# Performance work log

Hardware: AMD Instinct MI355X
Metric: run time of the kernel (lower is better)

## Reference

```python
import jax, jax.numpy as jnp
import numpy as np

B, S, V, D, F, H, L = 2, 1024, 32000, 768, 3072, 12, 6
DH = D // H


def layer_norm(x, g, b, eps=1e-5):
    mu = jnp.mean(x, axis=-1, keepdims=True)
    var = jnp.mean((x - mu) ** 2, axis=-1, keepdims=True)
    return (x - mu) / jnp.sqrt(var + eps) * g + b


def setup_inputs() -> dict:
    key = jax.random.key(0)
    ks = jax.random.split(key, 20)
    s = 0.02  # init scale
    p = {
        'x': jax.random.randint(ks[0], (B, S), 0, V),
        'tok_emb': jax.random.normal(ks[1], (V, D), jnp.float32) * s,
        'pos_emb': jax.random.normal(ks[2], (S, D), jnp.float32) * s,
        'Wq': jax.random.normal(ks[3], (L, D, D), jnp.float32) * s,
        'bq': jnp.zeros((L, D), jnp.float32),
        'Wk': jax.random.normal(ks[4], (L, D, D), jnp.float32) * s,
        'bk': jnp.zeros((L, D), jnp.float32),
        'Wv': jax.random.normal(ks[5], (L, D, D), jnp.float32) * s,
        'bv': jnp.zeros((L, D), jnp.float32),
        'Wo': jax.random.normal(ks[6], (L, D, D), jnp.float32) * s,
        'bo': jnp.zeros((L, D), jnp.float32),
        'ln1_g': jnp.ones((L, D), jnp.float32),
        'ln1_b': jnp.zeros((L, D), jnp.float32),
        'W1': jax.random.normal(ks[7], (L, D, F), jnp.float32) * s,
        'b1': jnp.zeros((L, F), jnp.float32),
        'W2': jax.random.normal(ks[8], (L, F, D), jnp.float32) * s,
        'b2': jnp.zeros((L, D), jnp.float32),
        'ln2_g': jnp.ones((L, D), jnp.float32),
        'ln2_b': jnp.zeros((L, D), jnp.float32),
        'Wf': jax.random.normal(ks[9], (D, V), jnp.float32) * s,
        'bf': jnp.zeros((V,), jnp.float32),
    }
    return p


def reference(x, tok_emb, pos_emb, Wq, bq, Wk, bk, Wv, bv, Wo, bo,
              ln1_g, ln1_b, W1, b1, W2, b2, ln2_g, ln2_b, Wf, bf):
    hset = tok_emb[x] + pos_emb[None, :x.shape[1], :]  # [B,S,D]
    scale = 1.0 / jnp.sqrt(jnp.float32(D))  # note: original scales by sqrt(d_k)=sqrt(d_model)
    for i in range(L):
        q = (hset @ Wq[i] + bq[i]).reshape(B, S, H, DH).transpose(0, 2, 1, 3)
        k = (hset @ Wk[i] + bk[i]).reshape(B, S, H, DH).transpose(0, 2, 1, 3)
        v = (hset @ Wv[i] + bv[i]).reshape(B, S, H, DH).transpose(0, 2, 1, 3)
        scores = jnp.einsum('bhqd,bhkd->bhqk', q, k) * scale
        probs = jax.nn.softmax(scores, axis=-1)
        o = jnp.einsum('bhqk,bhkd->bhqd', probs, v)
        o = o.transpose(0, 2, 1, 3).reshape(B, S, D)
        attn = o @ Wo[i] + bo[i]
        h1 = layer_norm(attn + hset, ln1_g[i], ln1_b[i])
        ff = jax.nn.gelu(h1 @ W1[i] + b1[i], approximate=False) @ W2[i] + b2[i]
        hset = layer_norm(ff + h1, ln2_g[i], ln2_b[i])
    logits = hset @ Wf + bf
    log_probs = jax.nn.log_softmax(logits, axis=-1)
    return (log_probs, hset)
```

## Files before the change

kernel.cpp:

```cpp
#include <hip/hip_runtime.h>
#include <hip/hip_bf16.h>
#include <math.h>

#define B_ 2
#define S_ 1024
#define V_ 32000
#define D_ 768
#define F_ 3072
#define H_ 12
#define L_ 6
#define DH_ 64
#define BS_ (B_*S_)
#define NQKV_ 2304
#define KVB_ 128

typedef __attribute__((ext_vector_type(8))) short short8;
typedef __attribute__((ext_vector_type(4))) float f32x4;

__device__ __forceinline__ unsigned short f2b(float f) {
    union { __hip_bfloat16 h; unsigned short u; } cv;
    cv.h = __float2bfloat16(f);
    return cv.u;
}

__device__ __forceinline__ void store_bf4(__hip_bfloat16* p, float a, float b, float c, float d) {
    unsigned long long pk = (unsigned long long)f2b(a)
        | ((unsigned long long)f2b(b) << 16)
        | ((unsigned long long)f2b(c) << 32)
        | ((unsigned long long)f2b(d) << 48);
    *(unsigned long long*)p = pk;
}

__device__ __forceinline__ void gld16(const void* g, void* l) {
    __builtin_amdgcn_global_load_lds(
        (const __attribute__((address_space(1))) unsigned int*)g,
        (__attribute__((address_space(3))) unsigned int*)l,
        16, 0, 0);
}

__global__ void embed_k(const int* __restrict__ x, const float* __restrict__ tok,
                        const float* __restrict__ pos, float* __restrict__ h,
                        __hip_bfloat16* __restrict__ hbf) {
    int bs = blockIdx.x;
    int s = bs % S_;
    int t = x[bs];
    for (int d = threadIdx.x; d < D_; d += blockDim.x) {
        float v = tok[(size_t)t * D_ + d] + pos[(size_t)s * D_ + d];
        h[(size_t)bs * D_ + d] = v;
        hbf[(size_t)bs * D_ + d] = __float2bfloat16(v);
    }
}

__global__ __launch_bounds__(256) void transp_k(const float* __restrict__ src, size_t sl,
                                                __hip_bfloat16* __restrict__ dst, size_t dl,
                                                int N, int K) {
    const float* S = src + (size_t)blockIdx.z * sl;
    __hip_bfloat16* Dp = dst + (size_t)blockIdx.z * dl;
    __shared__ float T[32][33];
    const int k0 = blockIdx.y * 32, n0 = blockIdx.x * 32;
    const int tid = threadIdx.x;
    const int r = tid >> 3, c4 = (tid & 7) * 4;
    float4 vv = *(const float4*)&S[(size_t)(k0 + r) * N + n0 + c4];
    T[r][c4 + 0] = vv.x; T[r][c4 + 1] = vv.y; T[r][c4 + 2] = vv.z; T[r][c4 + 3] = vv.w;
    __syncthreads();
    store_bf4(&Dp[(size_t)(n0 + r) * K + k0 + c4],
              T[c4 + 0][r], T[c4 + 1][r], T[c4 + 2][r], T[c4 + 3][r]);
}

__global__ void bcat_k(const float* __restrict__ bq, const float* __restrict__ bk,
                       const float* __restrict__ bv, float* __restrict__ dst) {
    int l = blockIdx.x;
    for (int j = threadIdx.x; j < D_; j += blockDim.x) {
        dst[(size_t)l * NQKV_ + j]          = bq[(size_t)l * D_ + j];
        dst[(size_t)l * NQKV_ + D_ + j]     = bk[(size_t)l * D_ + j];
        dst[(size_t)l * NQKV_ + 2 * D_ + j] = bv[(size_t)l * D_ + j];
    }
}

__global__ void cvt_k(const float* __restrict__ in, __hip_bfloat16* __restrict__ out, int n) {
    int i = (blockIdx.x * 256 + threadIdx.x) * 4;
    if (i < n) {
        float4 v = *(const float4*)&in[i];
        store_bf4(&out[i], v.x, v.y, v.z, v.w);
    }
}

template<int BM, int BN, int ACT, bool WF32, bool WBF, bool SW, bool XS, bool WVT>
__global__ __launch_bounds__(256) void mgemm_k(const __hip_bfloat16* __restrict__ A,
                                               const __hip_bfloat16* __restrict__ Bt,
                                               const float* __restrict__ bias,
                                               float* __restrict__ Cf,
                                               __hip_bfloat16* __restrict__ Cb,
                                               __hip_bfloat16* __restrict__ vTp,
                                               int M, int N, int K) {
    constexpr int WM = BM / 2, WN = BN / 2;
    constexpr int FM = WM / 16, FN = WN / 16;
    __shared__ __hip_bfloat16 Al[BM * 64];
    __shared__ __hip_bfloat16 Bl[BN * 64];
    const int tid = threadIdx.x;
    const int wid = tid >> 6, lane = tid & 63;
    const int wr = wid >> 1, wc = wid & 1;
    const int lrow = lane & 15, kq = lane >> 4;

    int bx = blockIdx.x, by = blockIdx.y;
    if (XS) {
        const int gx = gridDim.x;
        const int nwg = gx * gridDim.y;
        const int lin = by * gx + bx;
        const int logical = (lin & 7) * (nwg >> 3) + (lin >> 3);
        bx = logical % gx;
        by = logical / gx;
    }
    const int row0 = (SW ? bx : by) * BM;
    const int col0 = (SW ? by : bx) * BN;

    f32x4 acc[FM][FN];
    #pragma unroll
    for (int i = 0; i < FM; ++i)
        #pragma unroll
        for (int j = 0; j < FN; ++j)
            acc[i][j] = (f32x4){0.f, 0.f, 0.f, 0.f};

    const int srow = (lane >> 3);
    const int scol = ((lane & 7) ^ srow) * 8;

    for (int kk = 0; kk < K; kk += 64) {
        #pragma unroll
        for (int i = 0; i < BM / 32; ++i)
            gld16(A + (size_t)(row0 + i * 32 + wid * 8 + srow) * K + kk + scol,
                  &Al[(i * 32 + wid * 8) * 64]);
        #pragma unroll
        for (int i = 0; i < BN / 32; ++i)
            gld16(Bt + (size_t)(col0 + i * 32 + wid * 8 + srow) * K + kk + scol,
                  &Bl[(i * 32 + wid * 8) * 64]);
        __syncthreads();

        #pragma unroll
        for (int kc = 0; kc < 2; ++kc) {
            short8 af[FM], bfr[FN];
            #pragma unroll
            for (int i = 0; i < FM; ++i) {
                const int row = wr * WM + i * 16 + lrow;
                af[i] = *(const short8*)((const char*)Al + row * 128
                          + ((kc * 64 + kq * 16) ^ ((row & 7) << 4)));
            }
            #pragma unroll
            for (int j = 0; j < FN; ++j) {
                const int row = wc * WN + j * 16 + lrow;
                bfr[j] = *(const short8*)((const char*)Bl + row * 128
                          + ((kc * 64 + kq * 16) ^ ((row & 7) << 4)));
            }
            #pragma unroll
            for (int i = 0; i < FM; ++i)
                #pragma unroll
                for (int j = 0; j < FN; ++j)
                    acc[i][j] = __builtin_amdgcn_mfma_f32_16x16x32_bf16(af[i], bfr[j], acc[i][j], 0, 0, 0);
        }
        __syncthreads();
    }

    #pragma unroll
    for (int i = 0; i < FM; ++i)
        #pragma unroll
        for (int j = 0; j < FN; ++j) {
            const int col = col0 + wc * WN + j * 16 + lrow;
            const float bv = bias[col];
            const int rowq = row0 + wr * WM + i * 16 + kq * 4;
            if (WVT && col >= 1536) {
                const int cv = col - 1536;
                const int bh = (rowq >> 10) * H_ + (cv >> 6);
                store_bf4(&vTp[((size_t)bh * DH_ + (cv & 63)) * S_ + (rowq & 1023)],
                          acc[i][j][0] + bv, acc[i][j][1] + bv,
                          acc[i][j][2] + bv, acc[i][j][3] + bv);
            } else {
                #pragma unroll
                for (int r = 0; r < 4; ++r) {
                    const int row = rowq + r;
                    float vv = acc[i][j][r] + bv;
                    if (ACT == 1) vv = 0.5f * vv * (1.0f + erff(vv * 0.70710678118654752f));
                    if (WF32) Cf[(size_t)row * N + col] = vv;
                    if (WBF)  Cb[(size_t)row * N + col] = __float2bfloat16(vv);
                }
            }
        }
}

__global__ __launch_bounds__(256) void gemm_k(const float* __restrict__ A,
                                              const float* __restrict__ W,
                                              const float* __restrict__ bias,
                                              float* __restrict__ Cout,
                                              int M, int N, int K) {
    __shared__ float As[64][16];
    __shared__ float Bs[16][64];
    const int tid = threadIdx.x;
    const int tx = tid & 15, ty = tid >> 4;
    const int row0 = blockIdx.y * 64, col0 = blockIdx.x * 64;
    float acc[4][4] = {};

    for (int kk = 0; kk < K; kk += 16) {
        #pragma unroll
        for (int it = 0; it < 4; ++it) {
            int idx = tid + it * 256;
            int m = idx >> 4, k = idx & 15;
            As[m][k] = A[(size_t)(row0 + m) * K + kk + k];
            int r = idx >> 6, c = idx & 63;
            Bs[r][c] = W[(size_t)(kk + r) * N + col0 + c];
        }
        __syncthreads();
        #pragma unroll
        for (int k = 0; k < 16; ++k) {
            float a[4], b[4];
            #pragma unroll
            for (int i = 0; i < 4; ++i) a[i] = As[ty * 4 + i][k];
            #pragma unroll
            for (int j = 0; j < 4; ++j) b[j] = Bs[k][tx * 4 + j];
            #pragma unroll
            for (int i = 0; i < 4; ++i)
                #pragma unroll
                for (int j = 0; j < 4; ++j)
                    acc[i][j] += a[i] * b[j];
        }
        __syncthreads();
    }

    #pragma unroll
    for (int i = 0; i < 4; ++i) {
        int r = row0 + ty * 4 + i;
        #pragma unroll
        for (int j = 0; j < 4; ++j) {
            int c = col0 + tx * 4 + j;
            Cout[(size_t)r * N + c] = acc[i][j] + bias[c];
        }
    }
}

__global__ __launch_bounds__(256) void fattn_k(const __hip_bfloat16* __restrict__ qkv,
                                               const __hip_bfloat16* __restrict__ vT,
                                               __hip_bfloat16* __restrict__ o) {
    const int qt0 = blockIdx.x * 64;
    const int bh = blockIdx.y;
    const int b = bh / H_, hh = bh % H_;
    const size_t rb = (size_t)b * S_;
    const int hoff = hh * DH_;

    __shared__ __hip_bfloat16 Ks[KVB_ * 64];
    __shared__ __hip_bfloat16 Vt[64 * KVB_];
    __shared__ __hip_bfloat16 Ps[64 * KVB_];

    const int tid = threadIdx.x;
    const int w = tid >> 6, lane = tid & 63;
    const int lr = lane & 15, lk = lane >> 4;

    short8 aq[2];
    {
        const int qrow = qt0 + w * 16 + lr;
        #pragma unroll
        for (int kc = 0; kc < 2; ++kc)
            aq[kc] = *(const short8*)&qkv[(rb + qrow) * NQKV_ + hoff + kc * 32 + lk * 8];
    }

    f32x4 oacc[4];
    float m_i[4], l_i[4];
    #pragma unroll
    for (int r = 0; r < 4; ++r) {
        oacc[r] = (f32x4){0.f, 0.f, 0.f, 0.f};
        m_i[r] = -1e30f;
        l_i[r] = 0.f;
    }

    const size_t vbase = (size_t)bh * DH_ * S_;

    for (int kt0 = 0; kt0 < S_; kt0 += KVB_) {
        __syncthreads();
        #pragma unroll
        for (int t = 0; t < 4; ++t) {
            const int r0 = w * 32 + t * 8;
            const int r = r0 + (lane >> 3);
            const int cs = (lane & 7) ^ ((r & 7) ^ ((r >> 3) & 7));
            gld16(&qkv[(rb + kt0 + r) * NQKV_ + D_ + hoff + cs * 8], &Ks[r0 * 64]);
        }
        #pragma unroll
        for (int t = 0; t < 4; ++t) {
            const int d0 = w * 16 + t * 4;
            const int d = d0 + (lane >> 4);
            const int cs = (lane & 15) ^ (d & 15);
            gld16(&vT[vbase + (size_t)d * S_ + kt0 + cs * 8], &Vt[d0 * 128]);
        }
        __syncthreads();

        f32x4 s[8];
        #pragma unroll
        for (int j = 0; j < 8; ++j) s[j] = (f32x4){0.f, 0.f, 0.f, 0.f};
        __builtin_amdgcn_s_setprio(1);
        #pragma unroll
        for (int kc = 0; kc < 2; ++kc) {
            #pragma unroll
            for (int j = 0; j < 8; ++j) {
                int kr = j * 16 + lr;
                short8 bk = *(const short8*)((const char*)Ks + kr * 128
                              + ((kc * 64 + lk * 16) ^ ((((kr & 7) ^ ((kr >> 3) & 7)) << 4))));
                s[j] = __builtin_amdgcn_mfma_f32_16x16x32_bf16(aq[kc], bk, s[j], 0, 0, 0);
            }
        }
        __builtin_amdgcn_s_setprio(0);
        #pragma unroll
        for (int j = 0; j < 8; ++j)
            #pragma unroll
            for (int r = 0; r < 4; ++r)
                s[j][r] *= 0.03608439182435161f;

        #pragma unroll
        for (int r = 0; r < 4; ++r) {
            float tmax = s[0][r];
            #pragma unroll
            for (int j = 1; j < 8; ++j) tmax = fmaxf(tmax, s[j][r]);
            #pragma unroll
            for (int off = 1; off <= 8; off <<= 1)
                tmax = fmaxf(tmax, __shfl_xor(tmax, off));
            float mnew = fmaxf(m_i[r], tmax);
            float corr = __expf(m_i[r] - mnew);
            m_i[r] = mnew;
            float psum = 0.f;
            const int prow = w * 16 + lk * 4 + r;
            #pragma unroll
            for (int j = 0; j < 8; ++j) {
                float p = __expf(s[j][r] - mnew);
                psum += p;
                *(__hip_bfloat16*)((char*)Ps + prow * 256
                    + (((j * 16 + lr) * 2) ^ ((prow & 15) << 4))) = __float2bfloat16(p);
            }
            #pragma unroll
            for (int off = 1; off <= 8; off <<= 1)
                psum += __shfl_xor(psum, off);
            l_i[r] = l_i[r] * corr + psum;
            #pragma unroll
            for (int jd = 0; jd < 4; ++jd) oacc[jd][r] *= corr;
        }

        __builtin_amdgcn_s_setprio(1);
        #pragma unroll
        for (int ks = 0; ks < 4; ++ks) {
            const int prow = w * 16 + lr;
            short8 pa = *(const short8*)((const char*)Ps + prow * 256
                          + ((ks * 64 + lk * 16) ^ ((prow & 15) << 4)));
            #pragma unroll
            for (int jd = 0; jd < 4; ++jd) {
                int vr = jd * 16 + lr;
                short8 vb = *(const short8*)((const char*)Vt + vr * 256
                              + ((ks * 64 + lk * 16) ^ ((vr & 15) << 4)));
                oacc[jd] = __builtin_amdgcn_mfma_f32_16x16x32_bf16(pa, vb, oacc[jd], 0, 0, 0);
            }
        }
        __builtin_amdgcn_s_setprio(0);
    }

    #pragma unroll
    for (int r = 0; r < 4; ++r) {
        float inv = 1.0f / l_i[r];
        const int row = qt0 + w * 16 + lk * 4 + r;
        #pragma unroll
        for (int jd = 0; jd < 4; ++jd)
            o[(rb + row) * (size_t)D_ + hoff + jd * 16 + lr] = __float2bfloat16(oacc[jd][r] * inv);
    }
}

__global__ __launch_bounds__(256) void addln_k(const float* __restrict__ a,
                                               const float* __restrict__ b,
                                               const float* __restrict__ g,
                                               const float* __restrict__ beta,
                                               float* __restrict__ out,
                                               __hip_bfloat16* __restrict__ out_bf) {
    const int r = blockIdx.x;
    const int tid = threadIdx.x;
    __shared__ float red[256];
    float xv[3];
    float s = 0.f;
    #pragma unroll
    for (int i = 0; i < 3; ++i) {
        int d = tid + i * 256;
        xv[i] = a[(size_t)r * D_ + d] + b[(size_t)r * D_ + d];
        s += xv[i];
    }
    red[tid] = s; __syncthreads();
    for (int st = 128; st > 0; st >>= 1) { if (tid < st) red[tid] += red[tid + st]; __syncthreads(); }
    float mu = red[0] * (1.0f / D_);
    __syncthreads();
    s = 0.f;
    #pragma unroll
    for (int i = 0; i < 3; ++i) { float dd = xv[i] - mu; s += dd * dd; }
    red[tid] = s; __syncthreads();
    for (int st = 128; st > 0; st >>= 1) { if (tid < st) red[tid] += red[tid + st]; __syncthreads(); }
    float rstd = rsqrtf(red[0] * (1.0f / D_) + 1e-5f);
    #pragma unroll
    for (int i = 0; i < 3; ++i) {
        int d = tid + i * 256;
        float v = (xv[i] - mu) * rstd * g[d] + beta[d];
        out[(size_t)r * D_ + d] = v;
        out_bf[(size_t)r * D_ + d] = __float2bfloat16(v);
    }
}

__global__ __launch_bounds__(256) void lsm_k(float* __restrict__ lp) {
    const int r = blockIdx.x;
    const int tid = threadIdx.x;
    __shared__ float rm[256], rl[256];
    float* row = lp + (size_t)r * V_;
    float mt = -1e30f, lt = 0.f;
    for (int i = tid * 4; i < V_; i += 1024) {
        float4 v = *(const float4*)&row[i];
        float c = fmaxf(fmaxf(v.x, v.y), fmaxf(v.z, v.w));
        if (c > mt) { lt *= __expf(mt - c); mt = c; }
        lt += __expf(v.x - mt) + __expf(v.y - mt) + __expf(v.z - mt) + __expf(v.w - mt);
    }
    rm[tid] = mt; rl[tid] = lt; __syncthreads();
    for (int st = 128; st > 0; st >>= 1) {
        if (tid < st) {
            float m2 = rm[tid + st], l2 = rl[tid + st];
            float M = fmaxf(rm[tid], m2);
            rl[tid] = rl[tid] * __expf(rm[tid] - M) + l2 * __expf(m2 - M);
            rm[tid] = M;
        }
        __syncthreads();
    }
    float sub = rm[0] + __logf(rl[0]);
    for (int i = tid * 4; i < V_; i += 1024) {
        float4 v = *(const float4*)&row[i];
        v.x -= sub; v.y -= sub; v.z -= sub; v.w -= sub;
        *(float4*)&row[i] = v;
    }
}

extern "C" void kernel_launch(void* const* d_in, const int* in_sizes, int n_in,
                              void* d_out, int out_size, void* d_ws, size_t ws_size,
                              hipStream_t stream) {
    const int*   x    = (const int*)  d_in[0];
    const float* tok  = (const float*)d_in[1];
    const float* pos  = (const float*)d_in[2];
    const float* Wq   = (const float*)d_in[3];
    const float* bq   = (const float*)d_in[4];
    const float* Wk   = (const float*)d_in[5];
    const float* bk   = (const float*)d_in[6];
    const float* Wv   = (const float*)d_in[7];
    const float* bv   = (const float*)d_in[8];
    const float* Wo   = (const float*)d_in[9];
    const float* bo   = (const float*)d_in[10];
    const float* ln1g = (const float*)d_in[11];
    const float* ln1b = (const float*)d_in[12];
    const float* W1   = (const float*)d_in[13];
    const float* b1   = (const float*)d_in[14];
    const float* W2   = (const float*)d_in[15];
    const float* b2   = (const float*)d_in[16];
    const float* ln2g = (const float*)d_in[17];
    const float* ln2b = (const float*)d_in[18];
    const float* Wf   = (const float*)d_in[19];
    const float* bff  = (const float*)d_in[20];

    float* out = (float*)d_out;
    const size_t HS = (size_t)BS_ * D_;

    __hip_bfloat16* qkv_bf = (__hip_bfloat16*)out;
    __hip_bfloat16* vT     = (__hip_bfloat16*)(out + 2359296);
    __hip_bfloat16* att_bf = (__hip_bfloat16*)(out + 4718592);
    float* tmp   = out + 5505024;
    float* h1    = out + 7077888;
    __hip_bfloat16* h1_bf  = (__hip_bfloat16*)(out + 8650752);
    __hip_bfloat16* ff_bf  = (__hip_bfloat16*)(out + 9437184);
    __hip_bfloat16* h_bf   = (__hip_bfloat16*)(out + 12582912);
    __hip_bfloat16* Wqkv_t = (__hip_bfloat16*)(out + 13369344);
    __hip_bfloat16* Wo_t   = (__hip_bfloat16*)(out + 18677760);
    __hip_bfloat16* W1_t   = (__hip_bfloat16*)(out + 20447232);
    __hip_bfloat16* W2_t   = (__hip_bfloat16*)(out + 27525120);
    float* bqkv  = out + 34603008;
    float* h     = out + (size_t)BS_ * V_;

    const bool ws_ok = ws_size >= (size_t)(24576000ULL * 2 + HS * 2);
    __hip_bfloat16* Wf_t   = (__hip_bfloat16*)d_ws;
    __hip_bfloat16* hbf_ws = (__hip_bfloat16*)((char*)d_ws + 49152000);

    const size_t DD = (size_t)D_ * D_, DF = (size_t)D_ * F_;
    const size_t QKVL = (size_t)NQKV_ * D_;
    transp_k<<<dim3(D_/32, D_/32, L_), 256, 0, stream>>>(Wq, DD, Wqkv_t,          QKVL, D_, D_);
    transp_k<<<dim3(D_/32, D_/32, L_), 256, 0, stream>>>(Wk, DD, Wqkv_t + DD,     QKVL, D_, D_);
    transp_k<<<dim3(D_/32, D_/32, L_), 256, 0, stream>>>(Wv, DD, Wqkv_t + 2 * DD, QKVL, D_, D_);
    transp_k<<<dim3(D_/32, D_/32, L_), 256, 0, stream>>>(Wo, DD, Wo_t,            DD,   D_, D_);
    transp_k<<<dim3(F_/32, D_/32, L_), 256, 0, stream>>>(W1, DF, W1_t,            DF,   F_, D_);
    transp_k<<<dim3(D_/32, F_/32, L_), 256, 0, stream>>>(W2, DF, W2_t,            DF,   D_, F_);
    bcat_k<<<L_, 256, 0, stream>>>(bq, bk, bv, bqkv);
    if (ws_ok)
        transp_k<<<dim3(V_/32, D_/32, 1), 256, 0, stream>>>(Wf, 0, Wf_t, 0, V_, D_);

    embed_k<<<BS_, 256, 0, stream>>>(x, tok, pos, h, h_bf);

    const dim3 gQKV(NQKV_/128, BS_/128);
    const dim3 gFF1(F_/128,    BS_/128);
    const dim3 gOUT(D_/128,    BS_/64);
    const dim3 gA(S_/64, B_*H_);
    for (int i = 0; i < L_; ++i) {
        mgemm_k<128,128,0,false,true,false,false,true><<<gQKV, 256, 0, stream>>>(
            h_bf, Wqkv_t + (size_t)i * QKVL, bqkv + (size_t)i * NQKV_, nullptr, qkv_bf, vT, BS_, NQKV_, D_);
        fattn_k<<<gA, 256, 0, stream>>>(qkv_bf, vT, att_bf);
        mgemm_k<64,128,0,true,false,false,false,false><<<gOUT, 256, 0, stream>>>(
            att_bf, Wo_t + (size_t)i * DD, bo + (size_t)i * D_, tmp, nullptr, nullptr, BS_, D_, D_);
        addln_k<<<BS_, 256, 0, stream>>>(tmp, h, ln1g + (size_t)i * D_, ln1b + (size_t)i * D_, h1, h1_bf);
        mgemm_k<128,128,1,false,true,false,false,false><<<gFF1, 256, 0, stream>>>(
            h1_bf, W1_t + (size_t)i * DF, b1 + (size_t)i * F_, nullptr, ff_bf, nullptr, BS_, F_, D_);
        mgemm_k<64,128,0,true,false,false,false,false><<<gOUT, 256, 0, stream>>>(
            ff_bf, W2_t + (size_t)i * DF, b2 + (size_t)i * D_, tmp, nullptr, nullptr, BS_, D_, F_);
        addln_k<<<BS_, 256, 0, stream>>>(tmp, h1, ln2g + (size_t)i * D_, ln2b + (size_t)i * D_, h, h_bf);
    }

    if (ws_ok) {
        cvt_k<<<(int)(HS / 1024), 256, 0, stream>>>(h, hbf_ws, (int)HS);
        mgemm_k<128,128,0,true,false,true,true,false><<<dim3(BS_/128, V_/128), 256, 0, stream>>>(
            hbf_ws, Wf_t, bff, out, nullptr, nullptr, BS_, V_, D_);
    } else {
        gemm_k<<<dim3(V_/64, BS_/64), 256, 0, stream>>>(h, Wf, bff, out, BS_, V_, D_);
    }
    lsm_k<<<BS_, 256, 0, stream>>>(out);
}
```

Measured before the change: 1.314 ms.

## Fuse log-softmax row statistics into vocab GEMM epilogue and drop bf16 convert

The final vocab projection GEMM now computes per-row max and sum-exp partials for each 128-column tile in its epilogue and writes them to workspace. A new lsm2_k kernel combines these partials and only does the subtract pass, so the separate statistics pass over the large logits buffer is skipped. The last layer norm writes its bf16 output straight into the workspace buffer, which removes the cvt_k launch. The GEMM epilogue gains extra shuffles, exp calls and a block sync, and the new path needs a larger workspace.

```diff
diff --git a/kernel.cpp b/kernel.cpp
--- a/kernel.cpp
+++ b/kernel.cpp
@@ -77,21 +77,14 @@
     }
 }
 
-__global__ void cvt_k(const float* __restrict__ in, __hip_bfloat16* __restrict__ out, int n) {
-    int i = (blockIdx.x * 256 + threadIdx.x) * 4;
-    if (i < n) {
-        float4 v = *(const float4*)&in[i];
-        store_bf4(&out[i], v.x, v.y, v.z, v.w);
-    }
-}
-
-template<int BM, int BN, int ACT, bool WF32, bool WBF, bool SW, bool XS, bool WVT>
+template<int BM, int BN, int ACT, bool WF32, bool WBF, bool SW, bool XS, bool WVT, bool PART>
 __global__ __launch_bounds__(256) void mgemm_k(const __hip_bfloat16* __restrict__ A,
                                                const __hip_bfloat16* __restrict__ Bt,
                                                const float* __restrict__ bias,
                                                float* __restrict__ Cf,
                                                __hip_bfloat16* __restrict__ Cb,
                                                __hip_bfloat16* __restrict__ vTp,
+                                               float2* __restrict__ prt,
                                                int M, int N, int K) {
     constexpr int WM = BM / 2, WN = BN / 2;
     constexpr int FM = WM / 16, FN = WN / 16;
@@ -159,30 +152,68 @@
         __syncthreads();
     }
 
-    #pragma unroll
-    for (int i = 0; i < FM; ++i)
-        #pragma unroll
-        for (int j = 0; j < FN; ++j) {
-            const int col = col0 + wc * WN + j * 16 + lrow;
-            const float bv = bias[col];
-            const int rowq = row0 + wr * WM + i * 16 + kq * 4;
-            if (WVT && col >= 1536) {
-                const int cv = col - 1536;
-                const int bh = (rowq >> 10) * H_ + (cv >> 6);
-                store_bf4(&vTp[((size_t)bh * DH_ + (cv & 63)) * S_ + (rowq & 1023)],
-                          acc[i][j][0] + bv, acc[i][j][1] + bv,
-                          acc[i][j][2] + bv, acc[i][j][3] + bv);
-            } else {
+    if constexpr (PART) {
+        __shared__ float MhS[2][BM];
+        __shared__ float LhS[2][BM];
+        #pragma unroll
+        for (int i = 0; i < FM; ++i)
+            #pragma unroll
+            for (int r = 0; r < 4; ++r) {
+                const int rowl = wr * WM + i * 16 + kq * 4 + r;
+                const int row = row0 + rowl;
+                float vals[FN];
+                float mloc = -1e30f;
                 #pragma unroll
-                for (int r = 0; r < 4; ++r) {
-                    const int row = rowq + r;
-                    float vv = acc[i][j][r] + bv;
-                    if (ACT == 1) vv = 0.5f * vv * (1.0f + erff(vv * 0.70710678118654752f));
-                    if (WF32) Cf[(size_t)row * N + col] = vv;
-                    if (WBF)  Cb[(size_t)row * N + col] = __float2bfloat16(vv);
+                for (int j = 0; j < FN; ++j) {
+                    const int col = col0 + wc * WN + j * 16 + lrow;
+                    vals[j] = acc[i][j][r] + bias[col];
+                    Cf[(size_t)row * N + col] = vals[j];
+                    mloc = fmaxf(mloc, vals[j]);
                 }
-            }
-        }
+                #pragma unroll
+                for (int off = 1; off <= 8; off <<= 1)
+                    mloc = fmaxf(mloc, __shfl_xor(mloc, off));
+                float lloc = 0.f;
+                #pragma unroll
+                for (int j = 0; j < FN; ++j) lloc += __expf(vals[j] - mloc);
+                #pragma unroll
+                for (int off = 1; off <= 8; off <<= 1)
+                    lloc += __shfl_xor(lloc, off);
+                if (lrow == 0) { MhS[wc][rowl] = mloc; LhS[wc][rowl] = lloc; }
+            }
+        __syncthreads();
+        if (tid < BM) {
+            float m0 = MhS[0][tid], m1 = MhS[1][tid];
+            float Mx = fmaxf(m0, m1);
+            float Lx = LhS[0][tid] * __expf(m0 - Mx) + LhS[1][tid] * __expf(m1 - Mx);
+            prt[(size_t)(row0 + tid) * (N >> 7) + (col0 >> 7)] = make_float2(Mx, Lx);
+        }
+    } else {
+        #pragma unroll
+        for (int i = 0; i < FM; ++i)
+            #pragma unroll
+            for (int j = 0; j < FN; ++j) {
+                const int col = col0 + wc * WN + j * 16 + lrow;
+                const float bv = bias[col];
+                const int rowq = row0 + wr * WM + i * 16 + kq * 4;
+                if (WVT && col >= 1536) {
+                    const int cv = col - 1536;
+                    const int bh = (rowq >> 10) * H_ + (cv >> 6);
+                    store_bf4(&vTp[((size_t)bh * DH_ + (cv & 63)) * S_ + (rowq & 1023)],
+                              acc[i][j][0] + bv, acc[i][j][1] + bv,
+                              acc[i][j][2] + bv, acc[i][j][3] + bv);
+                } else {
+                    #pragma unroll
+                    for (int r = 0; r < 4; ++r) {
+                        const int row = rowq + r;
+                        float vv = acc[i][j][r] + bv;
+                        if (ACT == 1) vv = 0.5f * vv * (1.0f + erff(vv * 0.70710678118654752f));
+                        if (WF32) Cf[(size_t)row * N + col] = vv;
+                        if (WBF)  Cb[(size_t)row * N + col] = __float2bfloat16(vv);
+                    }
+                }
+            }
+    }
 }
 
 __global__ __launch_bounds__(256) void gemm_k(const float* __restrict__ A,
@@ -423,6 +454,35 @@
         __syncthreads();
     }
     float sub = rm[0] + __logf(rl[0]);
+    for (int i = tid * 4; i < V_; i += 1024) {
+        float4 v = *(const float4*)&row[i];
+        v.x -= sub; v.y -= sub; v.z -= sub; v.w -= sub;
+        *(float4*)&row[i] = v;
+    }
+}
+
+__global__ __launch_bounds__(256) void lsm2_k(float* __restrict__ lp,
+                                              const float2* __restrict__ prt) {
+    const int r = blockIdx.x;
+    const int tid = threadIdx.x;
+    __shared__ float rm[256], rl[256];
+    float m = -1e30f, l = 0.f;
+    if (tid < V_ / 128) {
+        float2 p = prt[(size_t)r * (V_ / 128) + tid];
+        m = p.x; l = p.y;
+    }
+    rm[tid] = m; rl[tid] = l; __syncthreads();
+    for (int st = 128; st > 0; st >>= 1) {
+        if (tid < st) {
+            float m2 = rm[tid + st], l2 = rl[tid + st];
+            float M = fmaxf(rm[tid], m2);
+            rl[tid] = rl[tid] * __expf(rm[tid] - M) + l2 * __expf(m2 - M);
+            rm[tid] = M;
+        }
+        __syncthreads();
+    }
+    float sub = rm[0] + __logf(rl[0]);
+    float* row = lp + (size_t)r * V_;
     for (int i = tid * 4; i < V_; i += 1024) {
         float4 v = *(const float4*)&row[i];
         v.x -= sub; v.y -= sub; v.z -= sub; v.w -= sub;
@@ -473,9 +533,11 @@
     float* bqkv  = out + 34603008;
     float* h     = out + (size_t)BS_ * V_;
 
-    const bool ws_ok = ws_size >= (size_t)(24576000ULL * 2 + HS * 2);
+    const bool ws_ok  = ws_size >= 52297728ULL;
+    const bool ws_ok2 = ws_size >= 56393728ULL;
     __hip_bfloat16* Wf_t   = (__hip_bfloat16*)d_ws;
     __hip_bfloat16* hbf_ws = (__hip_bfloat16*)((char*)d_ws + 49152000);
+    float2* prt = (float2*)((char*)d_ws + 52297728);
 
     const size_t DD = (size_t)D_ * D_, DF = (size_t)D_ * F_;
     const size_t QKVL = (size_t)NQKV_ * D_;
@@ -496,25 +558,32 @@
     const dim3 gOUT(D_/128,    BS_/64);
     const dim3 gA(S_/64, B_*H_);
     for (int i = 0; i < L_; ++i) {
-        mgemm_k<128,128,0,false,true,false,false,true><<<gQKV, 256, 0, stream>>>(
-            h_bf, Wqkv_t + (size_t)i * QKVL, bqkv + (size_t)i * NQKV_, nullptr, qkv_bf, vT, BS_, NQKV_, D_);
+        mgemm_k<128,128,0,false,true,false,false,true,false><<<gQKV, 256, 0, stream>>>(
+            h_bf, Wqkv_t + (size_t)i * QKVL, bqkv + (size_t)i * NQKV_, nullptr, qkv_bf, vT, nullptr, BS_, NQKV_, D_);
         fattn_k<<<gA, 256, 0, stream>>>(qkv_bf, vT, att_bf);
-        mgemm_k<64,128,0,true,false,false,false,false><<<gOUT, 256, 0, stream>>>(
-            att_bf, Wo_t + (size_t)i * DD, bo + (size_t)i * D_, tmp, nullptr, nullptr, BS_, D_, D_);
+        mgemm_k<64,128,0,true,false,false,false,false,false><<<gOUT, 256, 0, stream>>>(
+            att_bf, Wo_t + (size_t)i * DD, bo + (size_t)i * D_, tmp, nullptr, nullptr, nullptr, BS_, D_, D_);
         addln_k<<<BS_, 256, 0, stream>>>(tmp, h, ln1g + (size_t)i * D_, ln1b + (size_t)i * D_, h1, h1_bf);
-        mgemm_k<128,128,1,false,true,false,false,false><<<gFF1, 256, 0, stream>>>(
-            h1_bf, W1_t + (size_t)i * DF, b1 + (size_t)i * F_, nullptr, ff_bf, nullptr, BS_, F_, D_);
-        mgemm_k<64,128,0,true,false,false,false,false><<<gOUT, 256, 0, stream>>>(
-            ff_bf, W2_t + (size_t)i * DF, b2 + (size_t)i * D_, tmp, nullptr, nullptr, BS_, D_, F_);
-        addln_k<<<BS_, 256, 0, stream>>>(tmp, h1, ln2g + (size_t)i * D_, ln2b + (size_t)i * D_, h, h_bf);
+        mgemm_k<128,128,1,false,true,false,false,false,false><<<gFF1, 256, 0, stream>>>(
+            h1_bf, W1_t + (size_t)i * DF, b1 + (size_t)i * F_, nullptr, ff_bf, nullptr, nullptr, BS_, F_, D_);
+        mgemm_k<64,128,0,true,false,false,false,false,false><<<gOUT, 256, 0, stream>>>(
+            ff_bf, W2_t + (size_t)i * DF, b2 + (size_t)i * D_, tmp, nullptr, nullptr, nullptr, BS_, D_, F_);
+        __hip_bfloat16* obf = (i == L_ - 1 && ws_ok) ? hbf_ws : h_bf;
+        addln_k<<<BS_, 256, 0, stream>>>(tmp, h1, ln2g + (size_t)i * D_, ln2b + (size_t)i * D_, h, obf);
     }
 
     if (ws_ok) {
-        cvt_k<<<(int)(HS / 1024), 256, 0, stream>>>(h, hbf_ws, (int)HS);
-        mgemm_k<128,128,0,true,false,true,true,false><<<dim3(BS_/128, V_/128), 256, 0, stream>>>(
-            hbf_ws, Wf_t, bff, out, nullptr, nullptr, BS_, V_, D_);
+        if (ws_ok2) {
+            mgemm_k<128,128,0,true,false,true,true,false,true><<<dim3(BS_/128, V_/128), 256, 0, stream>>>(
+                hbf_ws, Wf_t, bff, out, nullptr, nullptr, prt, BS_, V_, D_);
+            lsm2_k<<<BS_, 256, 0, stream>>>(out, prt);
+        } else {
+            mgemm_k<128,128,0,true,false,true,true,false,false><<<dim3(BS_/128, V_/128), 256, 0, stream>>>(
+                hbf_ws, Wf_t, bff, out, nullptr, nullptr, nullptr, BS_, V_, D_);
+            lsm_k<<<BS_, 256, 0, stream>>>(out);
+        }
     } else {
         gemm_k<<<dim3(V_/64, BS_/64), 256, 0, stream>>>(h, Wf, bff, out, BS_, V_, D_);
-    }
-    lsm_k<<<BS_, 256, 0, stream>>>(out);
-}
+        lsm_k<<<BS_, 256, 0, stream>>>(out);
+    }
+}
```

After: 1.346 ms. 2.5% more time.
